# Kernel optimization log

Measured on AMD Instinct MI355X. Metric: run time of the kernel, lower is better.

## Reference

```python
import jax, jax.numpy as jnp
import numpy as np

B, S, NX, NH = 4, 2048, 1024, 16
HD = NX // NH
MASKED_BIAS = -10000.0


def setup_inputs() -> dict:
    key = jax.random.key(0)
    k1, k2, k3 = jax.random.split(key, 3)
    x = jax.random.normal(k1, (B, S, NX), dtype=jnp.float32)
    w_attn = jax.random.normal(k2, (NX, 3 * NX), dtype=jnp.float32) * 0.02
    b_attn = jnp.zeros((3 * NX,), dtype=jnp.float32)
    w_proj = jax.random.normal(k3, (NX, NX), dtype=jnp.float32) * 0.02
    b_proj = jnp.zeros((NX,), dtype=jnp.float32)
    return {"x": x, "w_attn": w_attn, "b_attn": b_attn, "w_proj": w_proj, "b_proj": b_proj}


def reference(x, w_attn, b_attn, w_proj, b_proj):
    b, s, nx = x.shape
    # c_attn (HF Conv1D): y = x @ W + b
    qkv = x @ w_attn + b_attn                      # [b, s, 3*nx]
    q, k, v = jnp.split(qkv, 3, axis=-1)
    # split heads -> [b, h, s, d]
    q = q.reshape(b, s, NH, HD).transpose(0, 2, 1, 3)
    k = k.reshape(b, s, NH, HD).transpose(0, 2, 1, 3)
    v = v.reshape(b, s, NH, HD).transpose(0, 2, 1, 3)
    # scaled scores, scale by 1/sqrt(head_dim) since scale=True
    w = jnp.einsum('bhqd,bhkd->bhqk', q, k) / jnp.sqrt(jnp.asarray(HD, x.dtype))
    # tril causal mask (bias buffer slice for nd == ns == s)
    causal = jnp.tril(jnp.ones((s, s), dtype=bool))
    w = jnp.where(causal, w, jnp.asarray(MASKED_BIAS, w.dtype))
    w = jax.nn.softmax(w, axis=-1)
    a = jnp.einsum('bhqk,bhkd->bhqd', w, v)        # [b, h, s, d]
    # merge heads -> [b, s, nx]
    a = a.transpose(0, 2, 1, 3).reshape(b, s, nx)
    # c_proj
    a = a @ w_proj + b_proj
    return a
```

## Files before the change

kernel.cpp:

```cpp
#include <hip/hip_runtime.h>
#include <stdint.h>

#define BATCH 4
#define SEQ 2048
#define NX 1024
#define NHEAD 16
#define HDIM 64
#define NTOK (BATCH * SEQ)
#define QKV_LD (3 * NX)

typedef __bf16 bf16_t;
typedef __bf16 bf16x8 __attribute__((ext_vector_type(8)));
typedef __bf16 bf16x4 __attribute__((ext_vector_type(4)));
typedef float  f32x4  __attribute__((ext_vector_type(4)));

#define GLOAD_LDS16(g, l) __builtin_amdgcn_global_load_lds( \
    (const __attribute__((address_space(1))) void*)(g),     \
    (__attribute__((address_space(3))) void*)(l), 16, 0, 0)

#define MFMA16(a, b, c) __builtin_amdgcn_mfma_f32_16x16x32_bf16((a), (b), (c), 0, 0, 0)

#define WAIT_VM4_BAR() do { \
    asm volatile("s_waitcnt vmcnt(4) lgkmcnt(0)" ::: "memory"); \
    __builtin_amdgcn_s_barrier(); } while (0)
#define WAIT_VM0_BAR() do { \
    asm volatile("s_waitcnt vmcnt(0) lgkmcnt(0)" ::: "memory"); \
    __builtin_amdgcn_s_barrier(); } while (0)

__global__ __launch_bounds__(256) void k_cast_bf16(const float* __restrict__ in,
                                                   bf16_t* __restrict__ out, int n4) {
  int stride = gridDim.x * blockDim.x;
  for (int i = blockIdx.x * blockDim.x + threadIdx.x; i < n4; i += stride) {
    f32x4 v = ((const f32x4*)in)[i];
    bf16x4 o;
    o[0] = (bf16_t)v[0]; o[1] = (bf16_t)v[1];
    o[2] = (bf16_t)v[2]; o[3] = (bf16_t)v[3];
    ((bf16x4*)out)[i] = o;
  }
}

__global__ __launch_bounds__(256) void k_transpose_cast(const float* __restrict__ in,
                                                        bf16_t* __restrict__ out,
                                                        int K, int N) {
  __shared__ float tile[32][33];
  const int kb = blockIdx.x * 32, nb = blockIdx.y * 32;
  const int tx = threadIdx.x & 31;
  const int ty = (threadIdx.x >> 5) * 4;
#pragma unroll
  for (int i = 0; i < 4; i++)
    tile[ty + i][tx] = in[(size_t)(kb + ty + i) * N + nb + tx];
  __syncthreads();
#pragma unroll
  for (int i = 0; i < 4; i++)
    out[(size_t)(nb + ty + i) * K + kb + tx] = (bf16_t)tile[tx][ty + i];
}

__global__ __launch_bounds__(256) void k_vtrans(const bf16_t* __restrict__ qkv,
                                                bf16_t* __restrict__ vt) {
  __shared__ bf16_t tile[32][33];
  const int s0 = blockIdx.x * 32;
  const int d0 = blockIdx.y * 32;
  const int bh = blockIdx.z;
  const int b = bh >> 4, h = bh & 15;
  const bf16_t* src = qkv + (size_t)b * SEQ * QKV_LD + 2 * NX + h * HDIM;
  const int tx = threadIdx.x & 31;
  const int ty = (threadIdx.x >> 5) * 4;
#pragma unroll
  for (int i = 0; i < 4; i++)
    tile[ty + i][tx] = src[(size_t)(s0 + ty + i) * QKV_LD + d0 + tx];
  __syncthreads();
  bf16_t* dst = vt + (size_t)bh * HDIM * SEQ;
#pragma unroll
  for (int i = 0; i < 4; i++)
    dst[(size_t)(d0 + ty + i) * SEQ + s0 + tx] = tile[tx][ty + i];
}

template <int OUT_BF16>
__global__ __launch_bounds__(256) void k_gemm_bt(const bf16_t* __restrict__ A,
                                                 const bf16_t* __restrict__ Bt,
                                                 const float* __restrict__ bias,
                                                 void* __restrict__ Cout,
                                                 int M, int N, int K) {
  __shared__ __align__(16) bf16_t lsA[3][128 * 32];
  __shared__ __align__(16) bf16_t lsB[3][128 * 32];
  const int tid  = threadIdx.x;
  const int lane = tid & 63;
  const int wid  = tid >> 6;
  const int wr   = wid >> 1, wc = wid & 1;
  const int m0 = blockIdx.x * 128, n0 = blockIdx.y * 128;

  const int srow = tid >> 2;
  const int scol = ((tid & 3) ^ (srow & 3)) * 8;
  const bf16_t* Ap = A  + (size_t)(m0 + srow) * K + scol;
  const bf16_t* Bp = Bt + (size_t)(n0 + srow) * K + scol;
  const int wbase = (tid & ~63) * 8;

  f32x4 acc[4][4];
#pragma unroll
  for (int i = 0; i < 4; i++)
#pragma unroll
    for (int j = 0; j < 4; j++) acc[i][j] = (f32x4){0.f, 0.f, 0.f, 0.f};

  const int fr = lane & 15;
  const int g2 = lane >> 4;
  const int rslot = (g2 ^ (fr & 3)) * 8;

  auto stage = [&](int buf, int k0) {
    GLOAD_LDS16(Ap + k0,                  &lsA[buf][wbase]);
    GLOAD_LDS16(Ap + (size_t)64 * K + k0, &lsA[buf][2048 + wbase]);
    GLOAD_LDS16(Bp + k0,                  &lsB[buf][wbase]);
    GLOAD_LDS16(Bp + (size_t)64 * K + k0, &lsB[buf][2048 + wbase]);
  };

  const int nk = K >> 5;
  stage(0, 0);
  stage(1, 32);
  asm volatile("s_waitcnt vmcnt(4)" ::: "memory");
  __builtin_amdgcn_s_barrier();

  for (int kt = 0; kt < nk; kt++) {
    const int cur = kt % 3;
    if (kt + 2 < nk) stage((kt + 2) % 3, (kt + 2) * 32);
    bf16x8 af[4], bfr[4];
#pragma unroll
    for (int mf = 0; mf < 4; mf++)
      af[mf] = *(const bf16x8*)&lsA[cur][(wr * 64 + mf * 16 + fr) * 32 + rslot];
#pragma unroll
    for (int nf = 0; nf < 4; nf++)
      bfr[nf] = *(const bf16x8*)&lsB[cur][(wc * 64 + nf * 16 + fr) * 32 + rslot];
#pragma unroll
    for (int mf = 0; mf < 4; mf++)
#pragma unroll
      for (int nf = 0; nf < 4; nf++)
        acc[mf][nf] = MFMA16(af[mf], bfr[nf], acc[mf][nf]);
    if (kt + 1 < nk) {
      if (kt + 2 < nk) WAIT_VM4_BAR(); else WAIT_VM0_BAR();
    }
  }

  const int col = lane & 15, rb = (lane >> 4) * 4;
#pragma unroll
  for (int mf = 0; mf < 4; mf++) {
#pragma unroll
    for (int nf = 0; nf < 4; nf++) {
      const int gm = m0 + wr * 64 + mf * 16 + rb;
      const int gn = n0 + wc * 64 + nf * 16 + col;
      const float bv = bias[gn];
#pragma unroll
      for (int r = 0; r < 4; r++) {
        float v = acc[mf][nf][r] + bv;
        if (OUT_BF16)
          ((bf16_t*)Cout)[(size_t)(gm + r) * N + gn] = (bf16_t)v;
        else
          ((float*)Cout)[(size_t)(gm + r) * N + gn] = v;
      }
    }
  }
}

__global__ __launch_bounds__(256, 2) void k_attn(const bf16_t* __restrict__ qkv,
                                                 const bf16_t* __restrict__ vt,
                                                 bf16_t* __restrict__ attout) {
  __shared__ __align__(16) bf16_t lsK[3][64 * 64];
  __shared__ __align__(16) bf16_t lsV[3][64 * 64];
  const int tid = threadIdx.x, lane = tid & 63, w = tid >> 6;
  const int blk = blockIdx.x;
  const int xcd = blk & 7, idx = blk >> 3;
  const int bh  = xcd * 8 + (idx & 7);
  const int qsb = 7 - (idx >> 3);
  const int b = bh >> 4, h = bh & 15;
  const bf16_t* Qb  = qkv + (size_t)b * SEQ * QKV_LD + h * HDIM;
  const bf16_t* Kb  = Qb + NX;
  const bf16_t* Vtb = vt + (size_t)bh * HDIM * SEQ;

  const int fr = lane & 15, g2 = lane >> 4;
  const int kb8 = g2 * 8;
  const int permA = (fr & 3) + 8 * (fr >> 2);

  auto stage = [&](int buf, int kv0) {
#pragma unroll
    for (int s = 0; s < 2; s++) {
      const int i = w * 128 + s * 64 + lane;
      const int row = i >> 3, slot = i & 7;
      const int sk = (row & 3) | (((row >> 3) & 1) << 2);
      GLOAD_LDS16(Kb + (size_t)(kv0 + row) * QKV_LD + ((slot ^ sk) << 3),
                  &lsK[buf][(w * 128 + s * 64) * 8]);
      GLOAD_LDS16(Vtb + (size_t)row * SEQ + kv0 + ((slot ^ (row & 7)) << 3),
                  &lsV[buf][(w * 128 + s * 64) * 8]);
    }
  };

  const int wb = qsb * 256 + w * 64;
  const int kv_last = wb;
  const int nst = qsb * 4 + 4;

  bf16x8 bq[4][2];
#pragma unroll
  for (int g = 0; g < 4; g++)
#pragma unroll
    for (int kf = 0; kf < 2; kf++) {
      bf16x8 t = *(const bf16x8*)&Qb[(size_t)(wb + g * 16 + fr) * QKV_LD + kf * 32 + kb8];
#pragma unroll
      for (int jj = 0; jj < 8; jj++) t[jj] = (bf16_t)((float)t[jj] * 0.1803368801f);
      bq[g][kf] = t;
    }

  float l_run[4] = {0.f, 0.f, 0.f, 0.f};
  f32x4 o[4][4];
#pragma unroll
  for (int g = 0; g < 4; g++)
#pragma unroll
    for (int d = 0; d < 4; d++) o[g][d] = (f32x4){0.f, 0.f, 0.f, 0.f};

  stage(0, 0);
  stage(1, 64);
  asm volatile("s_waitcnt vmcnt(4)" ::: "memory");
  __builtin_amdgcn_s_barrier();

  for (int st = 0; st < nst; st++) {
    const int kv0 = st * 64;
    const int cur = st % 3;
    if (st + 2 < nst) stage((st + 2) % 3, (st + 2) * 64);
    if (kv0 <= kv_last) {
      bf16x8 ak[2][2][2];
#pragma unroll
      for (int sub = 0; sub < 2; sub++)
#pragma unroll
        for (int ab = 0; ab < 2; ab++)
#pragma unroll
          for (int kf = 0; kf < 2; kf++) {
            const int row = sub * 32 + ab * 4 + permA;
            const int sk = (row & 3) | (((row >> 3) & 1) << 2);
            const int c = kf * 4 + g2;
            ak[sub][ab][kf] = *(const bf16x8*)&lsK[cur][row * 64 + ((c ^ sk) << 3)];
          }
      bf16x8 vbf[4][2];
#pragma unroll
      for (int df = 0; df < 4; df++)
#pragma unroll
        for (int hh = 0; hh < 2; hh++) {
          const int row = df * 16 + fr;
          const int c = hh * 4 + g2;
          vbf[df][hh] = *(const bf16x8*)&lsV[cur][row * 64 + ((c ^ (row & 7)) << 3)];
        }
      const int masked = (kv0 == kv_last);
#pragma unroll
      for (int g = 0; g < 4; g++) {
        f32x4 sAB[2][2];
        __builtin_amdgcn_s_setprio(1);
#pragma unroll
        for (int sub = 0; sub < 2; sub++)
#pragma unroll
          for (int ab = 0; ab < 2; ab++) {
            f32x4 s0 = (f32x4){0.f, 0.f, 0.f, 0.f};
            s0 = MFMA16(ak[sub][ab][0], bq[g][0], s0);
            s0 = MFMA16(ak[sub][ab][1], bq[g][1], s0);
            sAB[sub][ab] = s0;
          }
        __builtin_amdgcn_s_setprio(0);
        float sv[16];
#pragma unroll
        for (int sub = 0; sub < 2; sub++)
#pragma unroll
          for (int r = 0; r < 4; r++) {
            sv[sub * 8 + r]     = sAB[sub][0][r];
            sv[sub * 8 + 4 + r] = sAB[sub][1][r];
          }
        if (masked) {
          const int q_abs = wb + g * 16 + fr;
#pragma unroll
          for (int sub = 0; sub < 2; sub++)
#pragma unroll
            for (int r = 0; r < 4; r++) {
              if (kv0 + sub * 32 + g2 * 8 + r     > q_abs) sv[sub * 8 + r]     = -1e30f;
              if (kv0 + sub * 32 + g2 * 8 + 4 + r > q_abs) sv[sub * 8 + 4 + r] = -1e30f;
            }
        }
        float tsum = 0.f;
        bf16_t pb[16];
#pragma unroll
        for (int jj = 0; jj < 16; jj++) {
          float pv = exp2f(sv[jj]);
          tsum += pv;
          pb[jj] = (bf16_t)pv;
        }
        l_run[g] += tsum;
        bf16x8 pa0, pa1;
#pragma unroll
        for (int jj = 0; jj < 8; jj++) { pa0[jj] = pb[jj]; pa1[jj] = pb[8 + jj]; }
        __builtin_amdgcn_s_setprio(1);
#pragma unroll
        for (int df = 0; df < 4; df++) {
          o[g][df] = MFMA16(pa0, vbf[df][0], o[g][df]);
          o[g][df] = MFMA16(pa1, vbf[df][1], o[g][df]);
        }
        __builtin_amdgcn_s_setprio(0);
      }
    }
    if (st + 1 < nst) {
      if (st + 2 < nst) WAIT_VM4_BAR(); else WAIT_VM0_BAR();
    }
  }

#pragma unroll
  for (int g = 0; g < 4; g++) {
    float lt = l_run[g];
    lt += __shfl_xor(lt, 16);
    lt += __shfl_xor(lt, 32);
    const float inv = 1.f / lt;
#pragma unroll
    for (int r = 0; r < 4; r++) {
      const float iv = __shfl(inv, g2 * 4 + r);
      const int tok = b * SEQ + wb + g * 16 + g2 * 4 + r;
#pragma unroll
      for (int df = 0; df < 4; df++)
        attout[(size_t)tok * NX + h * HDIM + df * 16 + fr] = (bf16_t)(o[g][df][r] * iv);
    }
  }
}

extern "C" void kernel_launch(void* const* d_in, const int* in_sizes, int n_in,
                              void* d_out, int out_size, void* d_ws, size_t ws_size,
                              hipStream_t stream) {
  const float* x      = (const float*)d_in[0];
  const float* w_attn = (const float*)d_in[1];
  const float* b_attn = (const float*)d_in[2];
  const float* w_proj = (const float*)d_in[3];
  const float* b_proj = (const float*)d_in[4];

  char* ws = (char*)d_ws;
  bf16_t* xb  = (bf16_t*)ws;
  bf16_t* qkv = (bf16_t*)(ws + (16u << 20));
  bf16_t* wab = (bf16_t*)(ws + (64u << 20));
  bf16_t* vt  = (bf16_t*)(ws + (64u << 20));
  bf16_t* wpb = (bf16_t*)(ws + (80u << 20));
  bf16_t* att = xb;

  k_cast_bf16<<<2048, 256, 0, stream>>>(x, xb, NTOK * NX / 4);
  k_transpose_cast<<<dim3(NX / 32, (3 * NX) / 32), 256, 0, stream>>>(w_attn, wab, NX, 3 * NX);
  k_gemm_bt<1><<<dim3(NTOK / 128, (3 * NX) / 128), 256, 0, stream>>>(
      xb, wab, b_attn, (void*)qkv, NTOK, 3 * NX, NX);
  k_vtrans<<<dim3(SEQ / 32, HDIM / 32, BATCH * NHEAD), 256, 0, stream>>>(qkv, vt);
  k_transpose_cast<<<dim3(NX / 32, NX / 32), 256, 0, stream>>>(w_proj, wpb, NX, NX);
  k_attn<<<BATCH * NHEAD * 8, 256, 0, stream>>>(qkv, vt, att);
  k_gemm_bt<0><<<dim3(NTOK / 128, NX / 128), 256, 0, stream>>>(
      att, wpb, b_proj, d_out, NTOK, NX, NX);
}
```

Before: 192.9 us.

## Add 256x256 eight-wave phased GEMM for QKV projection, simplify 128-tile GEMM

New measurement: 206.2 us. 1.07x slower.

```diff
diff --git a/kernel.cpp b/kernel.cpp
--- a/kernel.cpp
+++ b/kernel.cpp
@@ -75,14 +75,124 @@
     dst[(size_t)(d0 + ty + i) * SEQ + s0 + tx] = tile[tx][ty + i];
 }
 
+#define PHASE8(MH, NH, READA, STAGE, ENDWAIT) do {                              \
+    if (READA) {                                                                \
+      _Pragma("unroll") for (int mf = 0; mf < 4; mf++)                          \
+      _Pragma("unroll") for (int ks = 0; ks < 2; ks++)                          \
+        af[mf][ks] = *(const bf16x8*)&lsA[cur][((MH)*128 + wq*64 + mf*16 + fr)*64 \
+                         + (((ks*4 + g2) ^ (fr & 3)) << 3)];                    \
+    }                                                                           \
+    bf16x8 bfr[2][2];                                                           \
+    _Pragma("unroll") for (int nf = 0; nf < 2; nf++)                            \
+    _Pragma("unroll") for (int ks = 0; ks < 2; ks++)                            \
+      bfr[nf][ks] = *(const bf16x8*)&lsB[cur][((NH)*128 + wn*32 + nf*16 + fr)*64 \
+                         + (((ks*4 + g2) ^ (fr & 3)) << 3)];                    \
+    STAGE;                                                                      \
+    __builtin_amdgcn_s_barrier();                                               \
+    asm volatile("s_waitcnt lgkmcnt(0)" ::: "memory");                          \
+    __builtin_amdgcn_sched_barrier(0);                                          \
+    __builtin_amdgcn_s_setprio(1);                                              \
+    _Pragma("unroll") for (int mf = 0; mf < 4; mf++)                            \
+    _Pragma("unroll") for (int nf = 0; nf < 2; nf++)                            \
+    _Pragma("unroll") for (int ks = 0; ks < 2; ks++)                            \
+      acc[MH][NH][mf][nf] = MFMA16(af[mf][ks], bfr[nf][ks], acc[MH][NH][mf][nf]); \
+    __builtin_amdgcn_s_setprio(0);                                              \
+    ENDWAIT;                                                                    \
+    __builtin_amdgcn_s_barrier();                                               \
+  } while (0)
+
+__global__ __launch_bounds__(512, 2) void k_gemm8(const bf16_t* __restrict__ A,
+                                                  const bf16_t* __restrict__ Bt,
+                                                  const float* __restrict__ bias,
+                                                  bf16_t* __restrict__ Cout,
+                                                  int M, int N, int K) {
+  __shared__ __align__(16) bf16_t lsA[2][256 * 64];
+  __shared__ __align__(16) bf16_t lsB[2][256 * 64];
+  const int tid = threadIdx.x, lane = tid & 63, wid = tid >> 6;
+  const int wq = wid >> 2;
+  const int wn = wid & 3;
+  const int m0 = blockIdx.x * 256, n0 = blockIdx.y * 256;
+  const int fr = lane & 15, g2 = lane >> 4;
+
+  const int srow8 = lane >> 3, sslot = lane & 7;
+  const int sswz = (sslot ^ (srow8 & 3)) << 3;
+
+  const bf16_t* Ab = A + (size_t)m0 * K;
+  const bf16_t* Bb = Bt + (size_t)n0 * K;
+
+  auto stA = [&](int buf, int half, int kt) {
+#pragma unroll
+    for (int i = 0; i < 2; i++) {
+      const int rl = half * 128 + (wid * 2 + i) * 8 + srow8;
+      GLOAD_LDS16(Ab + (size_t)rl * K + kt * 64 + sswz,
+                  &lsA[buf][(half * 128 + (wid * 2 + i) * 8) * 64]);
+    }
+  };
+  auto stB = [&](int buf, int half, int kt) {
+#pragma unroll
+    for (int i = 0; i < 2; i++) {
+      const int rl = half * 128 + (wid * 2 + i) * 8 + srow8;
+      GLOAD_LDS16(Bb + (size_t)rl * K + kt * 64 + sswz,
+                  &lsB[buf][(half * 128 + (wid * 2 + i) * 8) * 64]);
+    }
+  };
+
+  f32x4 acc[2][2][4][2];
+#pragma unroll
+  for (int a = 0; a < 2; a++)
+#pragma unroll
+    for (int b2 = 0; b2 < 2; b2++)
+#pragma unroll
+      for (int c = 0; c < 4; c++)
+#pragma unroll
+        for (int d = 0; d < 2; d++) acc[a][b2][c][d] = (f32x4){0.f, 0.f, 0.f, 0.f};
+
+  const int NT = K >> 6;
+  stA(0, 0, 0); stB(0, 0, 0); stA(0, 1, 0); stB(0, 1, 0);
+  stA(1, 0, 1); stB(1, 0, 1); stA(1, 1, 1);
+  asm volatile("s_waitcnt vmcnt(6)" ::: "memory");
+  __builtin_amdgcn_s_barrier();
+
+  bf16x8 af[4][2];
+  for (int t = 0; t < NT; t++) {
+    const int cur = t & 1, nxt = cur ^ 1;
+    PHASE8(0, 0, 1, { if (t + 1 < NT) stB(nxt, 1, t + 1); }, {});
+    PHASE8(0, 1, 0, { if (t + 2 < NT) stA(cur, 0, t + 2); }, {});
+    PHASE8(1, 0, 1, {}, {});
+    PHASE8(1, 1, 0,
+           { if (t + 2 < NT) { stB(cur, 0, t + 2); stA(cur, 1, t + 2); } },
+           { if (t < NT - 1) {
+               if (t == NT - 2) asm volatile("s_waitcnt vmcnt(0)" ::: "memory");
+               else             asm volatile("s_waitcnt vmcnt(6)" ::: "memory");
+             } });
+  }
+
+  const int col = lane & 15, rb = (lane >> 4) * 4;
+#pragma unroll
+  for (int mh = 0; mh < 2; mh++)
+#pragma unroll
+    for (int nh = 0; nh < 2; nh++)
+#pragma unroll
+      for (int mf = 0; mf < 4; mf++)
+#pragma unroll
+        for (int nf = 0; nf < 2; nf++) {
+          const int gm = m0 + mh * 128 + wq * 64 + mf * 16 + rb;
+          const int gn = n0 + nh * 128 + wn * 32 + nf * 16 + col;
+          const float bv = bias[gn];
+#pragma unroll
+          for (int r = 0; r < 4; r++)
+            Cout[(size_t)(gm + r) * N + gn] = (bf16_t)(acc[mh][nh][mf][nf][r] + bv);
+        }
+}
+
 template <int OUT_BF16>
 __global__ __launch_bounds__(256) void k_gemm_bt(const bf16_t* __restrict__ A,
                                                  const bf16_t* __restrict__ Bt,
                                                  const float* __restrict__ bias,
                                                  void* __restrict__ Cout,
                                                  int M, int N, int K) {
-  __shared__ __align__(16) bf16_t lsA[3][128 * 32];
-  __shared__ __align__(16) bf16_t lsB[3][128 * 32];
+  __shared__ __align__(16) bf16_t lsA[2][128 * 32];
+  __shared__ __align__(16) bf16_t lsB[2][128 * 32];
   const int tid  = threadIdx.x;
   const int lane = tid & 63;
   const int wid  = tid >> 6;
@@ -90,7 +200,7 @@
   const int m0 = blockIdx.x * 128, n0 = blockIdx.y * 128;
 
   const int srow = tid >> 2;
-  const int scol = ((tid & 3) ^ (srow & 3)) * 8;
+  const int scol = (tid & 3) * 8;
   const bf16_t* Ap = A  + (size_t)(m0 + srow) * K + scol;
   const bf16_t* Bp = Bt + (size_t)(n0 + srow) * K + scol;
   const int wbase = (tid & ~63) * 8;
@@ -102,8 +212,7 @@
     for (int j = 0; j < 4; j++) acc[i][j] = (f32x4){0.f, 0.f, 0.f, 0.f};
 
   const int fr = lane & 15;
-  const int g2 = lane >> 4;
-  const int rslot = (g2 ^ (fr & 3)) * 8;
+  const int kb = (lane >> 4) * 8;
 
   auto stage = [&](int buf, int k0) {
     GLOAD_LDS16(Ap + k0,                  &lsA[buf][wbase]);
@@ -112,30 +221,25 @@
     GLOAD_LDS16(Bp + (size_t)64 * K + k0, &lsB[buf][2048 + wbase]);
   };
 
+  stage(0, 0);
+  __syncthreads();
   const int nk = K >> 5;
-  stage(0, 0);
-  stage(1, 32);
-  asm volatile("s_waitcnt vmcnt(4)" ::: "memory");
-  __builtin_amdgcn_s_barrier();
-
   for (int kt = 0; kt < nk; kt++) {
-    const int cur = kt % 3;
-    if (kt + 2 < nk) stage((kt + 2) % 3, (kt + 2) * 32);
+    const int cur = kt & 1;
+    if (kt + 1 < nk) stage(cur ^ 1, (kt + 1) * 32);
     bf16x8 af[4], bfr[4];
 #pragma unroll
     for (int mf = 0; mf < 4; mf++)
-      af[mf] = *(const bf16x8*)&lsA[cur][(wr * 64 + mf * 16 + fr) * 32 + rslot];
+      af[mf] = *(const bf16x8*)&lsA[cur][(wr * 64 + mf * 16 + fr) * 32 + kb];
 #pragma unroll
     for (int nf = 0; nf < 4; nf++)
-      bfr[nf] = *(const bf16x8*)&lsB[cur][(wc * 64 + nf * 16 + fr) * 32 + rslot];
+      bfr[nf] = *(const bf16x8*)&lsB[cur][(wc * 64 + nf * 16 + fr) * 32 + kb];
 #pragma unroll
     for (int mf = 0; mf < 4; mf++)
 #pragma unroll
       for (int nf = 0; nf < 4; nf++)
         acc[mf][nf] = MFMA16(af[mf], bfr[nf], acc[mf][nf]);
-    if (kt + 1 < nk) {
-      if (kt + 2 < nk) WAIT_VM4_BAR(); else WAIT_VM0_BAR();
-    }
+    __syncthreads();
   }
 
   const int col = lane & 15, rb = (lane >> 4) * 4;
@@ -338,8 +442,8 @@
 
   k_cast_bf16<<<2048, 256, 0, stream>>>(x, xb, NTOK * NX / 4);
   k_transpose_cast<<<dim3(NX / 32, (3 * NX) / 32), 256, 0, stream>>>(w_attn, wab, NX, 3 * NX);
-  k_gemm_bt<1><<<dim3(NTOK / 128, (3 * NX) / 128), 256, 0, stream>>>(
-      xb, wab, b_attn, (void*)qkv, NTOK, 3 * NX, NX);
+  k_gemm8<<<dim3(NTOK / 256, (3 * NX) / 256), 512, 0, stream>>>(
+      xb, wab, b_attn, qkv, NTOK, 3 * NX, NX);
   k_vtrans<<<dim3(SEQ / 32, HDIM / 32, BATCH * NHEAD), 256, 0, stream>>>(qkv, vt);
   k_transpose_cast<<<dim3(NX / 32, NX / 32), 256, 0, stream>>>(w_proj, wpb, NX, NX);
   k_attn<<<BATCH * NHEAD * 8, 256, 0, stream>>>(qkv, vt, att);
```
